# Performance work log

Hardware: AMD Instinct MI355X
Metric: run time of the kernel (lower is better)

Reference implementation:

```python
import jax, jax.numpy as jnp
import numpy as np

S = 2        # downscale
REDUCE = 32  # QK channel dim


def _to_grid(x):
    # [B,C,H,W] -> [B,C,H/S,W/S,S*S], matching ConverToGrid (reshape+permute+reshape)
    B, C, H, W = x.shape
    h, w = H // S, W // S
    x = x.reshape(B, C, h, S, w, S)
    x = x.transpose(0, 1, 2, 4, 3, 5)
    return x.reshape(B, C, h, w, S * S)


def setup_inputs() -> dict:
    key = jax.random.key(0)
    k1, k2, k3 = jax.random.split(key, 3)
    fm = jax.random.normal(k1, (8, 128, 256, 256), dtype=jnp.float32)
    Wq = jax.random.normal(k2, (REDUCE, 128), dtype=jnp.float32) * 0.05
    Wk = jax.random.normal(k3, (REDUCE, 128), dtype=jnp.float32) * 0.05
    return {"fm": fm, "Wq": Wq, "Wk": Wk}


def reference(fm, Wq, Wk):
    B, C, H, W = fm.shape
    h, w = H // S, W // S
    # Q branch: AvgPool2d(S,S) -> 1x1 conv -> scale by 1/sqrt(reduce)
    pooled = fm.reshape(B, C, h, S, w, S).mean(axis=(3, 5))          # [B,C,h,w]
    Q = jnp.einsum('rc,bchw->brhw', Wq, pooled) / jnp.sqrt(
        jnp.asarray(REDUCE, fm.dtype))                               # [B,r,h,w]
    # K branch: 1x1 conv -> grid
    K = _to_grid(jnp.einsum('rc,bchw->brhw', Wk, fm))                # [B,r,h,w,S*S]
    # V branch: grid of raw features
    V = _to_grid(fm)                                                 # [B,C,h,w,S*S]
    # sum over channel dim of Q*K, softmax over window dim (dropout p=0 => identity)
    logits = jnp.einsum('brhw,brhws->bhws', Q, K)                    # [B,h,w,S*S]
    attn = jax.nn.softmax(logits, axis=-1)
    # weighted sum over window positions
    out = jnp.einsum('bchws,bhws->bchw', V, attn)                    # [B,C,h,w]
    return out
```

## Files before the change

### kernel.cpp

```cpp
#include <hip/hip_runtime.h>
#include <math.h>


__global__ __launch_bounds__(256) void wt_kernel(const float* __restrict__ Wq,
                                                 const float* __restrict__ Wk,
                                                 float* __restrict__ ws) {
  int t = blockIdx.x * 256 + threadIdx.x;
  if (t < 4096) {
    int c = t >> 5, r = t & 31;
    ws[c * 32 + r]        = Wq[r * 128 + c] * (0.25f / sqrtf(32.0f));
    ws[4096 + c * 32 + r] = Wk[r * 128 + c];
  }
}

__global__ __launch_bounds__(256, 4)
void attn_main(const float* __restrict__ fm,
               const float* __restrict__ ws,
               float* __restrict__ out) {
  __shared__ float Qpart[2 * 32 * 128];
  __shared__ float lbuf[2 * 128 * 4];
  __shared__ float abuf[128 * 4];

  const int tid  = threadIdx.x;
  const int p    = tid & 127;
  const int half = __builtin_amdgcn_readfirstlane(tid >> 7);
  const int blk  = blockIdx.x;
  const int h    = blk & 127;
  const int b    = blk >> 7;
  const int cbase = half * 64;

  const float* gbase = fm + ((size_t)(b * 128 + cbase) * 65536) +
                       (size_t)(2 * h) * 256 + 2 * p;
  const float* wq = ws + cbase * 32;
  const float* wk = ws + 4096 + cbase * 32;

  float qa[32];
#pragma unroll
  for (int r = 0; r < 32; ++r) qa[r] = 0.f;
  {
    const float* g = gbase;
#pragma unroll 4
    for (int i = 0; i < 64; ++i) {
      const float2 va = *(const float2*)(g);
      const float2 vb = *(const float2*)(g + 256);
      const float u = (va.x + va.y) + (vb.x + vb.y);
#pragma unroll
      for (int r = 0; r < 32; ++r)
        qa[r] = fmaf(wq[i * 32 + r], u, qa[r]);
      g += 65536;
    }
  }
#pragma unroll
  for (int r = 0; r < 32; ++r) Qpart[half * 4096 + r * 128 + p] = qa[r];
  __syncthreads();
#pragma unroll
  for (int r = 0; r < 32; ++r) qa[r] += Qpart[(half ^ 1) * 4096 + r * 128 + p];

  float l0 = 0.f, l1 = 0.f, l2 = 0.f, l3 = 0.f;
  {
    const float* g = gbase;
#pragma unroll 2
    for (int i = 0; i < 64; ++i) {
      const float2 va = *(const float2*)(g);
      const float2 vb = *(const float2*)(g + 256);
      float t0 = 0.f, t1 = 0.f, t2 = 0.f, t3 = 0.f;
#pragma unroll
      for (int r = 0; r < 32; r += 4) {
        t0 = fmaf(qa[r + 0], wk[i * 32 + r + 0], t0);
        t1 = fmaf(qa[r + 1], wk[i * 32 + r + 1], t1);
        t2 = fmaf(qa[r + 2], wk[i * 32 + r + 2], t2);
        t3 = fmaf(qa[r + 3], wk[i * 32 + r + 3], t3);
      }
      const float tv = (t0 + t1) + (t2 + t3);
      l0 = fmaf(tv, va.x, l0);
      l1 = fmaf(tv, va.y, l1);
      l2 = fmaf(tv, vb.x, l2);
      l3 = fmaf(tv, vb.y, l3);
      g += 65536;
    }
  }
  *(float4*)(lbuf + (half * 128 + p) * 4) = make_float4(l0, l1, l2, l3);
  __syncthreads();

  if (half == 0) {
    const float4 o = *(const float4*)(lbuf + (128 + p) * 4);
    const float L0 = l0 + o.x, L1 = l1 + o.y, L2 = l2 + o.z, L3 = l3 + o.w;
    const float mx = fmaxf(fmaxf(L0, L1), fmaxf(L2, L3));
    const float e0 = __expf(L0 - mx), e1 = __expf(L1 - mx);
    const float e2 = __expf(L2 - mx), e3 = __expf(L3 - mx);
    const float inv = 1.0f / ((e0 + e1) + (e2 + e3));
    *(float4*)(abuf + p * 4) =
        make_float4(e0 * inv, e1 * inv, e2 * inv, e3 * inv);
  }
  __syncthreads();
  const float4 at = *(const float4*)(abuf + p * 4);

  {
    const float* g = gbase;
    float* op = out + ((size_t)(b * 128 + cbase) * 16384) + h * 128 + p;
#pragma unroll 4
    for (int i = 0; i < 64; ++i) {
      const float2 va = *(const float2*)(g);
      const float2 vb = *(const float2*)(g + 256);
      *op = fmaf(at.x, va.x, fmaf(at.y, va.y, fmaf(at.z, vb.x, at.w * vb.y)));
      g += 65536;
      op += 16384;
    }
  }
}

extern "C" void kernel_launch(void* const* d_in, const int* in_sizes, int n_in,
                              void* d_out, int out_size, void* d_ws, size_t ws_size,
                              hipStream_t stream) {
  const float* fm = (const float*)d_in[0];
  const float* Wq = (const float*)d_in[1];
  const float* Wk = (const float*)d_in[2];
  float* outp = (float*)d_out;
  float* ws = (float*)d_ws;

  wt_kernel<<<16, 256, 0, stream>>>(Wq, Wk, ws);
  attn_main<<<1024, 256, 0, stream>>>(fm, ws, outp);
}
```

Before: 149.3 us.

## Shrink LDS, raise occupancy, reverse second pass for cache reuse, nontemporal stores

The Q-partial exchange now uses a single shared buffer, and the softmax weights reuse lbuf, which lowers LDS use so the launch bound can target 8 blocks per CU. The second pass over fm walks the channels in reverse so that the most recently loaded rows are read first while they are still in cache. The output loop is unrolled more and uses nontemporal stores to avoid polluting cache with output. The cost is an extra barrier for the Q exchange, and register pressure may rise or spill under the tighter bound.

```diff
diff --git a/kernel.cpp b/kernel.cpp
--- a/kernel.cpp
+++ b/kernel.cpp
@@ -13,13 +13,12 @@
   }
 }
 
-__global__ __launch_bounds__(256, 4)
+__global__ __launch_bounds__(256, 8)
 void attn_main(const float* __restrict__ fm,
                const float* __restrict__ ws,
                float* __restrict__ out) {
-  __shared__ float Qpart[2 * 32 * 128];
+  __shared__ float Qpart[32 * 128];
   __shared__ float lbuf[2 * 128 * 4];
-  __shared__ float abuf[128 * 4];
 
   const int tid  = threadIdx.x;
   const int p    = tid & 127;
@@ -50,17 +49,30 @@
       g += 65536;
     }
   }
+  if (half == 1) {
 #pragma unroll
-  for (int r = 0; r < 32; ++r) Qpart[half * 4096 + r * 128 + p] = qa[r];
+    for (int r = 0; r < 32; ++r) Qpart[r * 128 + p] = qa[r];
+  }
   __syncthreads();
+  if (half == 0) {
 #pragma unroll
-  for (int r = 0; r < 32; ++r) qa[r] += Qpart[(half ^ 1) * 4096 + r * 128 + p];
+    for (int r = 0; r < 32; ++r) {
+      const float t = qa[r] + Qpart[r * 128 + p];
+      qa[r] = t;
+      Qpart[r * 128 + p] = t;
+    }
+  }
+  __syncthreads();
+  if (half == 1) {
+#pragma unroll
+    for (int r = 0; r < 32; ++r) qa[r] = Qpart[r * 128 + p];
+  }
 
   float l0 = 0.f, l1 = 0.f, l2 = 0.f, l3 = 0.f;
   {
-    const float* g = gbase;
+    const float* g = gbase + (size_t)63 * 65536;
 #pragma unroll 2
-    for (int i = 0; i < 64; ++i) {
+    for (int i = 63; i >= 0; --i) {
       const float2 va = *(const float2*)(g);
       const float2 vb = *(const float2*)(g + 256);
       float t0 = 0.f, t1 = 0.f, t2 = 0.f, t3 = 0.f;
@@ -76,7 +88,7 @@
       l1 = fmaf(tv, va.y, l1);
       l2 = fmaf(tv, vb.x, l2);
       l3 = fmaf(tv, vb.y, l3);
-      g += 65536;
+      g -= 65536;
     }
   }
   *(float4*)(lbuf + (half * 128 + p) * 4) = make_float4(l0, l1, l2, l3);
@@ -89,20 +101,22 @@
     const float e0 = __expf(L0 - mx), e1 = __expf(L1 - mx);
     const float e2 = __expf(L2 - mx), e3 = __expf(L3 - mx);
     const float inv = 1.0f / ((e0 + e1) + (e2 + e3));
-    *(float4*)(abuf + p * 4) =
+    *(float4*)(lbuf + p * 4) =
         make_float4(e0 * inv, e1 * inv, e2 * inv, e3 * inv);
   }
   __syncthreads();
-  const float4 at = *(const float4*)(abuf + p * 4);
+  const float4 at = *(const float4*)(lbuf + p * 4);
 
   {
     const float* g = gbase;
     float* op = out + ((size_t)(b * 128 + cbase) * 16384) + h * 128 + p;
-#pragma unroll 4
+#pragma unroll 8
     for (int i = 0; i < 64; ++i) {
       const float2 va = *(const float2*)(g);
       const float2 vb = *(const float2*)(g + 256);
-      *op = fmaf(at.x, va.x, fmaf(at.y, va.y, fmaf(at.z, vb.x, at.w * vb.y)));
+      const float o =
+          fmaf(at.x, va.x, fmaf(at.y, va.y, fmaf(at.z, vb.x, at.w * vb.y)));
+      __builtin_nontemporal_store(o, op);
       g += 65536;
       op += 16384;
     }
```

Result: no change. 149.0 us (-0.2%).
